# Kernel optimization log

Measured on AMD Instinct MI355X. Metric: run time of the kernel, lower is better.

Reference implementation:

```python
import jax, jax.numpy as jnp
import numpy as np

B, SW, SS, D, H = 2, 1024, 256, 1024, 16  # D = hidden_dim*num_heads = 64*16


def _dense_init(key, d_in, d_out):
    # xavier_uniform kernel, zero bias
    lim = np.sqrt(6.0 / (d_in + d_out))
    k = jax.random.uniform(key, (d_in, d_out), jnp.float32, -lim, lim)
    b = jnp.zeros((d_out,), jnp.float32)
    return k, b


def setup_inputs() -> dict:
    key = jax.random.key(0)
    ks = jax.random.split(key, 16)
    inp = {
        'word_inputs': jax.random.normal(ks[0], (B, SW, D), jnp.float32),
        'word_context': jax.random.normal(ks[1], (B, SW, D), jnp.float32),
        'sentence_inputs': jax.random.normal(ks[2], (B, SS, D), jnp.float32),
        'sentence_context': jax.random.normal(ks[3], (B, SS, D), jnp.float32),
        'word_mask': jax.random.uniform(ks[4], (B, H, SW, SW), jnp.float32),
        'sentence_mask': jax.random.uniform(ks[5], (B, H, SS, SS), jnp.float32),
    }
    names = ['wq', 'wk', 'wv', 'wo', 'sq', 'sk', 'sv', 'so']
    for i, n in enumerate(names):
        kk, bb = _dense_init(ks[6 + i], D, D)
        inp[n + '_k'] = kk
        inp[n + '_b'] = bb
    return inp


def _attention(q, k, v, mask):
    # Faithful to source: split heads by raw reshape (B, H, L, hd),
    # scale by sqrt(full key dim), multiplicative mask.
    Bq, Lk, Dm = v.shape[0], v.shape[1], q.shape[-1]
    hd = Dm // H
    qh = jnp.reshape(q, (Bq, H, Lk, hd))
    kh = jnp.reshape(k, (Bq, H, Lk, hd))
    vh = jnp.reshape(v, (Bq, H, Lk, hd))
    scores = jnp.einsum('bhqd,bhkd->bhqk', qh, kh) / jnp.sqrt(jnp.float32(Dm))
    if mask is not None:
        scores = scores * mask
    attn = jax.nn.softmax(scores, axis=-1)
    ctx = jnp.einsum('bhqk,bhkd->bhqd', attn, vh)
    return attn, jnp.reshape(ctx, (Bq, Lk, Dm))


def reference(word_inputs, word_context, sentence_inputs, sentence_context,
              word_mask, sentence_mask,
              wq_k, wq_b, wk_k, wk_b, wv_k, wv_b, wo_k, wo_b,
              sq_k, sq_b, sk_k, sk_b, sv_k, sv_b, so_k, so_b):
    dense = lambda x, k, b: jnp.einsum('bld,de->ble', x, k) + b
    wq = dense(word_inputs, wq_k, wq_b)
    wk = dense(word_context, wk_k, wk_b)
    wv = dense(word_context, wv_k, wv_b)
    word_attn, word_ctx = _attention(wq, wk, wv, word_mask)
    sq = dense(sentence_inputs, sq_k, sq_b)
    sk = dense(sentence_context, sk_k, sk_b)
    sv = dense(sentence_context, sv_k, sv_b)
    sent_attn, sent_ctx = _attention(sq, sk, sv, sentence_mask)
    word_out = dense(word_ctx, wo_k, wo_b)
    sent_out = dense(sent_ctx, so_k, so_b)
    return (word_out, sent_out, word_attn, sent_attn)
```

## Files before the change

kernel.cpp:

```cpp
#include <hip/hip_runtime.h>
#include <hip/hip_bf16.h>
#include <stdint.h>

typedef __attribute__((ext_vector_type(8))) short short8;
typedef __attribute__((ext_vector_type(4))) float f32x4;

__device__ __forceinline__ f32x4 mfma16(short8 a, short8 b, f32x4 c){
  return __builtin_amdgcn_mfma_f32_16x16x32_bf16(a, b, c, 0, 0, 0);
}

union BF8 { short8 v; __hip_bfloat16 h[8]; };

__device__ __forceinline__ void gld_lds16(const void* g, void* l){
  __builtin_amdgcn_global_load_lds((const __attribute__((address_space(1))) void*)g,
                                   (__attribute__((address_space(3))) void*)l, 16, 0, 0);
}

struct GemmDesc { const __hip_bfloat16* A; const __hip_bfloat16* W; const float* bias; void* out; int M; float scale; };
struct GemmArgs { GemmDesc d[6]; };
struct PrepWArgs { const float* src[8]; };
struct CvtArgs { const float* src[4]; __hip_bfloat16* dst[4]; int n[4]; };

__global__ __launch_bounds__(256) void cvt_k(CvtArgs c){
  int z = blockIdx.z;
  int n = c.n[z];
  int i = (blockIdx.x * 256 + threadIdx.x) * 8;
  if (i >= n) return;
  const float4* s = (const float4*)(c.src[z] + i);
  float4 u0 = s[0], u1 = s[1];
  BF8 cv;
  cv.h[0] = __float2bfloat16(u0.x); cv.h[1] = __float2bfloat16(u0.y);
  cv.h[2] = __float2bfloat16(u0.z); cv.h[3] = __float2bfloat16(u0.w);
  cv.h[4] = __float2bfloat16(u1.x); cv.h[5] = __float2bfloat16(u1.y);
  cv.h[6] = __float2bfloat16(u1.z); cv.h[7] = __float2bfloat16(u1.w);
  *(short8*)(c.dst[z] + i) = cv.v;
}

__global__ __launch_bounds__(256) void prep_w_k(PrepWArgs pa, __hip_bfloat16* dst){
  __shared__ float t[64][65];
  const float* W = pa.src[blockIdx.z];
  int k0 = blockIdx.y * 64, n0 = blockIdx.x * 64;
  int c = threadIdx.x & 63, r0 = (threadIdx.x >> 6) * 16;
  #pragma unroll
  for (int i = 0; i < 16; ++i) t[r0 + i][c] = W[(size_t)(k0 + r0 + i) * 1024 + n0 + c];
  __syncthreads();
  __hip_bfloat16* D = dst + (size_t)blockIdx.z * 1048576;
  #pragma unroll
  for (int i = 0; i < 16; ++i) D[(size_t)(n0 + r0 + i) * 1024 + k0 + c] = __float2bfloat16(t[c][r0 + i]);
}

__global__ __launch_bounds__(256) void prep_v_k(const __hip_bfloat16* vw, const __hip_bfloat16* vs,
                                                __hip_bfloat16* vtw, __hip_bfloat16* vts){
  bool word = (blockIdx.z == 0);
  int L = word ? 1024 : 256;
  if (!word && blockIdx.x >= 4) return;
  __shared__ __hip_bfloat16 t[64][65];
  const __hip_bfloat16* src = (word ? vw : vs) + (size_t)blockIdx.y * L * 64;
  __hip_bfloat16* dst = (word ? vtw : vts) + (size_t)blockIdx.y * L * 64;
  int l0 = blockIdx.x * 64;
  int c = threadIdx.x & 63, r0 = (threadIdx.x >> 6) * 16;
  #pragma unroll
  for (int i = 0; i < 16; ++i) t[r0 + i][c] = src[(size_t)(l0 + r0 + i) * 64 + c];
  __syncthreads();
  #pragma unroll
  for (int i = 0; i < 16; ++i) dst[(size_t)(r0 + i) * L + l0 + c] = t[c][r0 + i];
}

template<bool OUT_BF16>
__global__ __launch_bounds__(256) void gemm_k(GemmArgs ga){
  GemmDesc dd = ga.d[blockIdx.z];
  int m0 = blockIdx.y * 128;
  if (m0 >= dd.M) return;
  int n0 = blockIdx.x * 128;

  __shared__ __align__(16) __hip_bfloat16 lA[2][128 * 32];
  __shared__ __align__(16) __hip_bfloat16 lB[2][128 * 32];

  int tid = threadIdx.x, lane = tid & 63, wv = tid >> 6;
  int r16 = lane & 15, g = lane >> 4;
  int wr = wv >> 1, wc = wv & 1;

  const __hip_bfloat16* Ab = dd.A + (size_t)m0 * 1024;
  const __hip_bfloat16* Wb = dd.W + (size_t)n0 * 1024;
  int lrow = lane >> 2;
  int scol = (lane & 3) * 8;

  #define STAGE(buf, kc)                                                            \
    {                                                                               \
      _Pragma("unroll")                                                             \
      for (int h = 0; h < 2; ++h){                                                  \
        int rbase = h * 64 + wv * 16;                                               \
        int row = rbase + lrow;                                                     \
        gld_lds16(Ab + (size_t)row * 1024 + (kc) + scol, &lA[buf][rbase * 32]);     \
        gld_lds16(Wb + (size_t)row * 1024 + (kc) + scol, &lB[buf][rbase * 32]);     \
      }                                                                             \
    }

  f32x4 acc[4][4] = {};
  STAGE(0, 0);
  int cur = 0;
  for (int kc = 0; kc < 1024; kc += 32){
    if (kc + 32 < 1024) STAGE(cur ^ 1, kc + 32);
    __syncthreads();
    const __hip_bfloat16* la = &lA[cur][(wr * 64) * 32];
    const __hip_bfloat16* lb = &lB[cur][(wc * 64) * 32];
    short8 af[4], bfr[4];
    #pragma unroll
    for (int t = 0; t < 4; ++t){
      af[t]  = *(const short8*)(la + (t * 16 + r16) * 32 + g * 8);
      bfr[t] = *(const short8*)(lb + (t * 16 + r16) * 32 + g * 8);
    }
    #pragma unroll
    for (int mt = 0; mt < 4; ++mt)
      #pragma unroll
      for (int nt = 0; nt < 4; ++nt)
        acc[mt][nt] = mfma16(af[mt], bfr[nt], acc[mt][nt]);
    __syncthreads();
    cur ^= 1;
  }
  #undef STAGE

  #pragma unroll
  for (int nt = 0; nt < 4; ++nt){
    int col = n0 + wc * 64 + nt * 16 + r16;
    float bb = dd.bias[col];
    #pragma unroll
    for (int mt = 0; mt < 4; ++mt){
      int row0 = m0 + wr * 64 + mt * 16 + g * 4;
      #pragma unroll
      for (int r = 0; r < 4; ++r){
        float v = (acc[mt][nt][r] + bb) * dd.scale;
        if (OUT_BF16) ((__hip_bfloat16*)dd.out)[(size_t)(row0 + r) * 1024 + col] = __float2bfloat16(v);
        else          ((float*)dd.out)[(size_t)(row0 + r) * 1024 + col] = v;
      }
    }
  }
}

template<int L>
__global__ __launch_bounds__(512, 2) void attn_k(
    const __hip_bfloat16* __restrict__ qb, const __hip_bfloat16* __restrict__ kb,
    const __hip_bfloat16* __restrict__ vt, const float* __restrict__ mask,
    float* __restrict__ attn, __hip_bfloat16* __restrict__ ctx){
  constexpr int HALF = L / 2, KT = HALF / 16, CH = HALF / 32;
  int bh = blockIdx.y;
  int q0 = blockIdx.x * 64;
  int lane = threadIdx.x & 63, wv = threadIdx.x >> 6;
  int qt = wv >> 1, hf = wv & 1;
  int r16 = lane & 15, g = lane >> 4;
  size_t ho = (size_t)bh * L * 64;
  const __hip_bfloat16* Qp = qb + ho;
  const __hip_bfloat16* Kp = kb + ho + (size_t)hf * HALF * 64;
  const __hip_bfloat16* Vp = vt + ho;
  int q = q0 + qt * 16 + r16;
  const float* mrow = mask + (size_t)bh * L * L + (size_t)q * L + hf * HALF;
  float* arow = attn + (size_t)bh * L * L + (size_t)q * L + hf * HALF;

  short8 qf0 = *(const short8*)(Qp + (size_t)q * 64 + g * 8);
  short8 qf1 = *(const short8*)(Qp + (size_t)q * 64 + 32 + g * 8);

  f32x4 s[KT];
  #pragma unroll
  for (int kt = 0; kt < KT; ++kt){
    const __hip_bfloat16* kr = Kp + (size_t)(kt * 16 + r16) * 64 + g * 8;
    short8 kf0 = *(const short8*)kr;
    short8 kf1 = *(const short8*)(kr + 32);
    f32x4 t = {};
    t = mfma16(kf0, qf0, t);
    t = mfma16(kf1, qf1, t);
    int kbase = kt * 16 + g * 4;
    #pragma unroll
    for (int r = 0; r < 4; ++r) t[r] *= mrow[kbase + r];
    s[kt] = t;
  }

  float mx = -3.0e38f;
  #pragma unroll
  for (int kt = 0; kt < KT; ++kt)
    #pragma unroll
    for (int r = 0; r < 4; ++r) mx = fmaxf(mx, s[kt][r]);
  mx = fmaxf(mx, __shfl_xor(mx, 16));
  mx = fmaxf(mx, __shfl_xor(mx, 32));
  __shared__ float redm[4][2][16], redl[4][2][16];
  if (lane < 16) redm[qt][hf][lane] = mx;
  __syncthreads();
  mx = fmaxf(mx, redm[qt][1 ^ hf][r16]);
  float sm = 0.f;
  #pragma unroll
  for (int kt = 0; kt < KT; ++kt)
    #pragma unroll
    for (int r = 0; r < 4; ++r){ float e = __expf(s[kt][r] - mx); s[kt][r] = e; sm += e; }
  sm += __shfl_xor(sm, 16);
  sm += __shfl_xor(sm, 32);
  if (lane < 16) redl[qt][hf][lane] = sm;
  __syncthreads();
  sm += redl[qt][1 ^ hf][r16];
  float inv = 1.0f / sm;

  #pragma unroll
  for (int kt = 0; kt < KT; ++kt){
    int kbase = kt * 16 + g * 4;
    #pragma unroll
    for (int r = 0; r < 4; ++r){ float v = s[kt][r] * inv; s[kt][r] = v; arow[kbase + r] = v; }
  }

  __shared__ __align__(16) __hip_bfloat16 plds[8][16][40];
  f32x4 c4[4] = {};
  #pragma unroll
  for (int ch = 0; ch < CH; ++ch){
    asm volatile("s_waitcnt lgkmcnt(0)" ::: "memory");
    #pragma unroll
    for (int t = 0; t < 2; ++t){
      union { uint64_t u; __hip_bfloat16 h[4]; } pk;
      pk.h[0] = __float2bfloat16(s[2 * ch + t][0]);
      pk.h[1] = __float2bfloat16(s[2 * ch + t][1]);
      pk.h[2] = __float2bfloat16(s[2 * ch + t][2]);
      pk.h[3] = __float2bfloat16(s[2 * ch + t][3]);
      *(uint64_t*)&plds[wv][r16][t * 16 + g * 4] = pk.u;
    }
    asm volatile("s_waitcnt lgkmcnt(0)" ::: "memory");
    __builtin_amdgcn_sched_barrier(0);
    short8 pf = *(const short8*)&plds[wv][r16][g * 8];
    const __hip_bfloat16* vpp = Vp + hf * HALF + ch * 32 + g * 8;
    #pragma unroll
    for (int nt = 0; nt < 4; ++nt){
      short8 vf = *(const short8*)(vpp + (size_t)(nt * 16 + r16) * L);
      c4[nt] = mfma16(pf, vf, c4[nt]);
    }
  }

  __shared__ float ctxl[4][16][64];
  if (hf == 0){
    #pragma unroll
    for (int nt = 0; nt < 4; ++nt)
      #pragma unroll
      for (int r = 0; r < 4; ++r) ctxl[qt][g * 4 + r][nt * 16 + r16] = c4[nt][r];
  }
  __syncthreads();
  if (hf == 1){
    #pragma unroll
    for (int nt = 0; nt < 4; ++nt)
      #pragma unroll
      for (int r = 0; r < 4; ++r){
        float v = c4[nt][r] + ctxl[qt][g * 4 + r][nt * 16 + r16];
        ctx[ho + (size_t)(q0 + qt * 16 + g * 4 + r) * 64 + nt * 16 + r16] = __float2bfloat16(v);
      }
  }
}

extern "C" void kernel_launch(void* const* d_in, const int* in_sizes, int n_in,
                              void* d_out, int out_size, void* d_ws, size_t ws_size,
                              hipStream_t stream){
  const float* word_mask = (const float*)d_in[4];
  const float* sent_mask = (const float*)d_in[5];

  char* ws = (char*)d_ws;
  const size_t MB = 1048576;
  __hip_bfloat16* Wt   = (__hip_bfloat16*)(ws);
  __hip_bfloat16* bwi  = (__hip_bfloat16*)(ws + 16 * MB);
  __hip_bfloat16* bwc  = (__hip_bfloat16*)(ws + 20 * MB);
  __hip_bfloat16* bsi  = (__hip_bfloat16*)(ws + 24 * MB);
  __hip_bfloat16* bsc  = (__hip_bfloat16*)(ws + 25 * MB);
  __hip_bfloat16* qw   = (__hip_bfloat16*)(ws + 26 * MB);
  __hip_bfloat16* kw   = (__hip_bfloat16*)(ws + 30 * MB);
  __hip_bfloat16* vw   = (__hip_bfloat16*)(ws + 34 * MB);
  __hip_bfloat16* sqb  = (__hip_bfloat16*)(ws + 38 * MB);
  __hip_bfloat16* skb  = (__hip_bfloat16*)(ws + 39 * MB);
  __hip_bfloat16* svb  = (__hip_bfloat16*)(ws + 40 * MB);
  __hip_bfloat16* vtw  = (__hip_bfloat16*)(ws + 41 * MB);
  __hip_bfloat16* vts  = (__hip_bfloat16*)(ws + 45 * MB);
  __hip_bfloat16* ctxw = (__hip_bfloat16*)(ws + 46 * MB);
  __hip_bfloat16* ctxs = (__hip_bfloat16*)(ws + 50 * MB);

  float* out = (float*)d_out;
  float* word_out  = out;
  float* sent_out  = out + 2097152;
  float* word_attn = out + 2621440;
  float* sent_attn = out + 36175872;

  PrepWArgs pw;
  pw.src[0] = (const float*)d_in[6];  pw.src[1] = (const float*)d_in[8];
  pw.src[2] = (const float*)d_in[10]; pw.src[3] = (const float*)d_in[12];
  pw.src[4] = (const float*)d_in[14]; pw.src[5] = (const float*)d_in[16];
  pw.src[6] = (const float*)d_in[18]; pw.src[7] = (const float*)d_in[20];
  prep_w_k<<<dim3(16, 16, 8), 256, 0, stream>>>(pw, Wt);

  CvtArgs cv;
  cv.src[0] = (const float*)d_in[0]; cv.dst[0] = bwi; cv.n[0] = 2097152;
  cv.src[1] = (const float*)d_in[1]; cv.dst[1] = bwc; cv.n[1] = 2097152;
  cv.src[2] = (const float*)d_in[2]; cv.dst[2] = bsi; cv.n[2] = 524288;
  cv.src[3] = (const float*)d_in[3]; cv.dst[3] = bsc; cv.n[3] = 524288;
  cvt_k<<<dim3(1024, 1, 4), 256, 0, stream>>>(cv);

  GemmArgs g1;
  g1.d[0] = { bwi, Wt + (size_t)0 * 1048576, (const float*)d_in[7],  qw,  2048, 1.0f / 32.0f };
  g1.d[1] = { bwc, Wt + (size_t)1 * 1048576, (const float*)d_in[9],  kw,  2048, 1.0f };
  g1.d[2] = { bwc, Wt + (size_t)2 * 1048576, (const float*)d_in[11], vw,  2048, 1.0f };
  g1.d[3] = { bsi, Wt + (size_t)4 * 1048576, (const float*)d_in[15], sqb, 512,  1.0f / 32.0f };
  g1.d[4] = { bsc, Wt + (size_t)5 * 1048576, (const float*)d_in[17], skb, 512,  1.0f };
  g1.d[5] = { bsc, Wt + (size_t)6 * 1048576, (const float*)d_in[19], svb, 512,  1.0f };
  gemm_k<true><<<dim3(8, 16, 6), 256, 0, stream>>>(g1);

  prep_v_k<<<dim3(16, 32, 2), 256, 0, stream>>>(vw, svb, vtw, vts);

  attn_k<1024><<<dim3(16, 32), 512, 0, stream>>>(qw, kw, vtw, word_mask, word_attn, ctxw);
  attn_k<256><<<dim3(4, 32), 512, 0, stream>>>(sqb, skb, vts, sent_mask, sent_attn, ctxs);

  GemmArgs g2 = {};
  g2.d[0] = { ctxw, Wt + (size_t)3 * 1048576, (const float*)d_in[13], word_out, 2048, 1.0f };
  g2.d[1] = { ctxs, Wt + (size_t)7 * 1048576, (const float*)d_in[21], sent_out, 512,  1.0f };
  gemm_k<false><<<dim3(8, 16, 2), 256, 0, stream>>>(g2);
}
```

Measured before the change: 213.7 us.

## Split attention keys across four waves and vectorize mask/attn accesses

Each attention block now covers 32 queries, and four waves each take a quarter of the key range instead of two halves. This halves the per-wave score registers so occupancy can rise to three blocks per SM, and it doubles the grid. Mask loads and attention-probability stores become float4 accesses. The context partials are reduced through padded LDS by all waves with packed bf16 stores. In exchange there is more cross-wave reduction work and more LDS per block.

```diff
diff --git a/kernel.cpp b/kernel.cpp
--- a/kernel.cpp
+++ b/kernel.cpp
@@ -138,23 +138,23 @@
 }
 
 template<int L>
-__global__ __launch_bounds__(512, 2) void attn_k(
+__global__ __launch_bounds__(512, 3) void attn_k(
     const __hip_bfloat16* __restrict__ qb, const __hip_bfloat16* __restrict__ kb,
     const __hip_bfloat16* __restrict__ vt, const float* __restrict__ mask,
     float* __restrict__ attn, __hip_bfloat16* __restrict__ ctx){
-  constexpr int HALF = L / 2, KT = HALF / 16, CH = HALF / 32;
+  constexpr int KQ = L / 4, KT = KQ / 16, CH = KQ / 32;
   int bh = blockIdx.y;
-  int q0 = blockIdx.x * 64;
+  int q0 = blockIdx.x * 32;
   int lane = threadIdx.x & 63, wv = threadIdx.x >> 6;
-  int qt = wv >> 1, hf = wv & 1;
+  int qt = wv >> 2, kq = wv & 3;
   int r16 = lane & 15, g = lane >> 4;
   size_t ho = (size_t)bh * L * 64;
   const __hip_bfloat16* Qp = qb + ho;
-  const __hip_bfloat16* Kp = kb + ho + (size_t)hf * HALF * 64;
+  const __hip_bfloat16* Kp = kb + ho + (size_t)kq * KQ * 64;
   const __hip_bfloat16* Vp = vt + ho;
   int q = q0 + qt * 16 + r16;
-  const float* mrow = mask + (size_t)bh * L * L + (size_t)q * L + hf * HALF;
-  float* arow = attn + (size_t)bh * L * L + (size_t)q * L + hf * HALF;
+  const float* mrow = mask + (size_t)bh * L * L + (size_t)q * L + kq * KQ;
+  float* arow = attn + (size_t)bh * L * L + (size_t)q * L + kq * KQ;
 
   short8 qf0 = *(const short8*)(Qp + (size_t)q * 64 + g * 8);
   short8 qf1 = *(const short8*)(Qp + (size_t)q * 64 + 32 + g * 8);
@@ -168,9 +168,8 @@
     f32x4 t = {};
     t = mfma16(kf0, qf0, t);
     t = mfma16(kf1, qf1, t);
-    int kbase = kt * 16 + g * 4;
-    #pragma unroll
-    for (int r = 0; r < 4; ++r) t[r] *= mrow[kbase + r];
+    float4 mv = *(const float4*)(mrow + kt * 16 + g * 4);
+    t[0] *= mv.x; t[1] *= mv.y; t[2] *= mv.z; t[3] *= mv.w;
     s[kt] = t;
   }
 
@@ -181,10 +180,11 @@
     for (int r = 0; r < 4; ++r) mx = fmaxf(mx, s[kt][r]);
   mx = fmaxf(mx, __shfl_xor(mx, 16));
   mx = fmaxf(mx, __shfl_xor(mx, 32));
-  __shared__ float redm[4][2][16], redl[4][2][16];
-  if (lane < 16) redm[qt][hf][lane] = mx;
-  __syncthreads();
-  mx = fmaxf(mx, redm[qt][1 ^ hf][r16]);
+  __shared__ float redm[2][4][16], redl[2][4][16];
+  if (lane < 16) redm[qt][kq][lane] = mx;
+  __syncthreads();
+  mx = fmaxf(fmaxf(redm[qt][0][r16], redm[qt][1][r16]),
+             fmaxf(redm[qt][2][r16], redm[qt][3][r16]));
   float sm = 0.f;
   #pragma unroll
   for (int kt = 0; kt < KT; ++kt)
@@ -192,16 +192,18 @@
     for (int r = 0; r < 4; ++r){ float e = __expf(s[kt][r] - mx); s[kt][r] = e; sm += e; }
   sm += __shfl_xor(sm, 16);
   sm += __shfl_xor(sm, 32);
-  if (lane < 16) redl[qt][hf][lane] = sm;
-  __syncthreads();
-  sm += redl[qt][1 ^ hf][r16];
+  if (lane < 16) redl[qt][kq][lane] = sm;
+  __syncthreads();
+  sm = (redl[qt][0][r16] + redl[qt][1][r16]) + (redl[qt][2][r16] + redl[qt][3][r16]);
   float inv = 1.0f / sm;
 
   #pragma unroll
   for (int kt = 0; kt < KT; ++kt){
-    int kbase = kt * 16 + g * 4;
-    #pragma unroll
-    for (int r = 0; r < 4; ++r){ float v = s[kt][r] * inv; s[kt][r] = v; arow[kbase + r] = v; }
+    float4 v;
+    v.x = s[kt][0] * inv; v.y = s[kt][1] * inv;
+    v.z = s[kt][2] * inv; v.w = s[kt][3] * inv;
+    s[kt][0] = v.x; s[kt][1] = v.y; s[kt][2] = v.z; s[kt][3] = v.w;
+    *(float4*)(arow + kt * 16 + g * 4) = v;
   }
 
   __shared__ __align__(16) __hip_bfloat16 plds[8][16][40];
@@ -221,7 +223,7 @@
     asm volatile("s_waitcnt lgkmcnt(0)" ::: "memory");
     __builtin_amdgcn_sched_barrier(0);
     short8 pf = *(const short8*)&plds[wv][r16][g * 8];
-    const __hip_bfloat16* vpp = Vp + hf * HALF + ch * 32 + g * 8;
+    const __hip_bfloat16* vpp = Vp + kq * KQ + ch * 32 + g * 8;
     #pragma unroll
     for (int nt = 0; nt < 4; ++nt){
       short8 vf = *(const short8*)(vpp + (size_t)(nt * 16 + r16) * L);
@@ -229,22 +231,22 @@
     }
   }
 
-  __shared__ float ctxl[4][16][64];
-  if (hf == 0){
-    #pragma unroll
-    for (int nt = 0; nt < 4; ++nt)
-      #pragma unroll
-      for (int r = 0; r < 4; ++r) ctxl[qt][g * 4 + r][nt * 16 + r16] = c4[nt][r];
-  }
-  __syncthreads();
-  if (hf == 1){
-    #pragma unroll
-    for (int nt = 0; nt < 4; ++nt)
-      #pragma unroll
-      for (int r = 0; r < 4; ++r){
-        float v = c4[nt][r] + ctxl[qt][g * 4 + r][nt * 16 + r16];
-        ctx[ho + (size_t)(q0 + qt * 16 + g * 4 + r) * 64 + nt * 16 + r16] = __float2bfloat16(v);
-      }
+  __shared__ float ctxl[2][4][16][65];
+  #pragma unroll
+  for (int nt = 0; nt < 4; ++nt)
+    #pragma unroll
+    for (int r = 0; r < 4; ++r) ctxl[qt][kq][g * 4 + r][nt * 16 + r16] = c4[nt][r];
+  __syncthreads();
+  {
+    int dq = kq * 16 + g * 4;
+    union { uint64_t u; __hip_bfloat16 h[4]; } ov;
+    #pragma unroll
+    for (int rr = 0; rr < 4; ++rr){
+      float v = (ctxl[qt][0][r16][dq + rr] + ctxl[qt][1][r16][dq + rr]) +
+                (ctxl[qt][2][r16][dq + rr] + ctxl[qt][3][r16][dq + rr]);
+      ov.h[rr] = __float2bfloat16(v);
+    }
+    *(uint64_t*)(ctx + ho + (size_t)(q0 + qt * 16 + r16) * 64 + dq) = ov.u;
   }
 }
 
@@ -303,8 +305,8 @@
 
   prep_v_k<<<dim3(16, 32, 2), 256, 0, stream>>>(vw, svb, vtw, vts);
 
-  attn_k<1024><<<dim3(16, 32), 512, 0, stream>>>(qw, kw, vtw, word_mask, word_attn, ctxw);
-  attn_k<256><<<dim3(4, 32), 512, 0, stream>>>(sqb, skb, vts, sent_mask, sent_attn, ctxs);
+  attn_k<1024><<<dim3(32, 32), 512, 0, stream>>>(qw, kw, vtw, word_mask, word_attn, ctxw);
+  attn_k<256><<<dim3(8, 32), 512, 0, stream>>>(sqb, skb, vts, sent_mask, sent_attn, ctxs);
 
   GemmArgs g2 = {};
   g2.d[0] = { ctxw, Wt + (size_t)3 * 1048576, (const float*)d_in[13], word_out, 2048, 1.0f };
```

New measurement: 200.4 us. 6.2% less time.
